# Optimization experiments

Measured on AMD Instinct MI355X. Metric: run time of the kernel, lower is better.

## Reference

```python
import jax, jax.numpy as jnp
import numpy as np

B, T, D, H = 2, 2048, 1024, 16
HD = D // H  # head dim = 64

def setup_inputs() -> dict:
    key = jax.random.key(0)
    k1, k2, k3 = jax.random.split(key, 3)
    x = jax.random.normal(k1, (B, T, D), dtype=jnp.float32)
    W_qkv = jax.random.normal(k2, (D, 3 * D), dtype=jnp.float32) * 0.02
    b_qkv = jax.random.normal(k3, (3 * D,), dtype=jnp.float32) * 0.02
    return {"x": x, "W_qkv": W_qkv, "b_qkv": b_qkv}

def reference(x, W_qkv, b_qkv):
    Bc, Tc, C = x.shape
    qkv = x @ W_qkv + b_qkv                     # [B,T,3D]
    q, k, v = jnp.split(qkv, 3, axis=-1)        # each [B,T,D]
    def to_heads(t):
        return t.reshape(Bc, Tc, H, HD).transpose(0, 2, 1, 3)  # [B,H,T,hd]
    q, k, v = to_heads(q), to_heads(k), to_heads(v)
    scale = 1.0 / jnp.sqrt(jnp.asarray(HD, dtype=x.dtype))
    att = jnp.einsum('bhqd,bhkd->bhqk', q, k) * scale  # [B,H,T,T]
    att = jax.nn.softmax(att, axis=-1)
    y = jnp.einsum('bhqk,bhkd->bhqd', att, v)          # [B,H,T,hd]
    return y.transpose(0, 2, 1, 3).reshape(Bc, Tc, C)
```

## Files before the change

### kernel.cpp

```cpp
#include <hip/hip_runtime.h>
#include <cstdint>

typedef unsigned short u16;
typedef __bf16 bf16x8 __attribute__((ext_vector_type(8)));
typedef float f32x4 __attribute__((ext_vector_type(4)));
typedef u16 u16x4 __attribute__((ext_vector_type(4)));
typedef u16 u16x8 __attribute__((ext_vector_type(8)));

static __device__ __forceinline__ u16 f2bf(float f) {
  return __builtin_bit_cast(u16, (__bf16)f);
}
static __device__ __forceinline__ float fexp2(float x) {
  float r;
  asm("v_exp_f32 %0, %1" : "=v"(r) : "v"(x));
  return r;
}

#define GLOAD16(gsrc, ldst) \
  __builtin_amdgcn_global_load_lds((const __attribute__((address_space(1))) void*)(gsrc), \
                                   (__attribute__((address_space(3))) void*)(ldst), 16, 0, 0)


__global__ __launch_bounds__(256) void k_prep(const float* __restrict__ x,
                                              const float* __restrict__ W,
                                              u16* __restrict__ xbf,
                                              u16* __restrict__ Wt) {
  __shared__ __align__(16) u16 tile[64 * 72];
  int t = threadIdx.x;
  if (blockIdx.x < 2048) {
    int idx = blockIdx.x * 256 + t;
    const float4* xv = (const float4*)x;
    float4 a = xv[(size_t)idx * 2];
    float4 b = xv[(size_t)idx * 2 + 1];
    u16x8 o;
    o[0]=f2bf(a.x); o[1]=f2bf(a.y); o[2]=f2bf(a.z); o[3]=f2bf(a.w);
    o[4]=f2bf(b.x); o[5]=f2bf(b.y); o[6]=f2bf(b.z); o[7]=f2bf(b.w);
    *(u16x8*)(xbf + (size_t)idx * 8) = o;
    return;
  }
  int bid = blockIdx.x - 2048;
  int bk = bid & 15, bn = bid >> 4;
  int k0 = bk * 64, n0 = bn * 64;
  #pragma unroll
  for (int r = 0; r < 4; r++) {
    int id = r * 256 + t;
    int kl = id >> 4;
    int c  = (id & 15) * 4;
    float4 v = *(const float4*)(W + (size_t)(k0 + kl) * 3072 + n0 + c);
    u16x4 o; o[0]=f2bf(v.x); o[1]=f2bf(v.y); o[2]=f2bf(v.z); o[3]=f2bf(v.w);
    *(u16x4*)(tile + kl * 72 + c) = o;
  }
  __syncthreads();
  #pragma unroll
  for (int r = 0; r < 2; r++) {
    int id = r * 256 + t;
    int nl = id >> 3;
    int w  = id & 7;
    u16x8 o;
    #pragma unroll
    for (int i = 0; i < 8; i++) o[i] = tile[(w * 8 + i) * 72 + nl];
    *(u16x8*)(Wt + (size_t)(n0 + nl) * 1024 + k0 + w * 8) = o;
  }
}

__global__ __launch_bounds__(256, 2) void k_gemm_qkv(const u16* __restrict__ xbf,
                                                     const u16* __restrict__ wt,
                                                     const float* __restrict__ bias,
                                                     u16* __restrict__ qkv,
                                                     u16* __restrict__ vT) {
  __shared__ __align__(16) u16 As[2 * 128 * 64];
  __shared__ __align__(16) u16 Bs[2 * 192 * 64];
  int wg = blockIdx.x;
  int swz = (wg & 7) * 64 + (wg >> 3);
  int mt = swz >> 4, nt = swz & 15;
  int m0 = mt * 128, n0 = nt * 192;
  int t = threadIdx.x;
  int lane = t & 63, wid = t >> 6;
  int wm = wid >> 1, wn = wid & 1;
  int g = lane >> 4, li = lane & 15;

  f32x4 acc[4][6];
  #pragma unroll
  for (int i = 0; i < 4; i++)
    #pragma unroll
    for (int j = 0; j < 6; j++) acc[i][j] = (f32x4){0.f, 0.f, 0.f, 0.f};

  auto stage = [&](int kt, int buf) {
    char* ad = (char*)As + buf * 16384;
    char* bd = (char*)Bs + buf * 24576;
    #pragma unroll
    for (int i = 0; i < 4; i++) {
      int p = t + i * 256;
      int row = p >> 3, ug = (p & 7) ^ (row & 7);
      GLOAD16(xbf + (size_t)(m0 + row) * 1024 + kt * 64 + ug * 8, ad + p * 16);
    }
    #pragma unroll
    for (int i = 0; i < 6; i++) {
      int p = t + i * 256;
      int row = p >> 3, ug = (p & 7) ^ (row & 7);
      GLOAD16(wt + (size_t)(n0 + row) * 1024 + kt * 64 + ug * 8, bd + p * 16);
    }
  };

  stage(0, 0);
  for (int kt = 0; kt < 16; ++kt) {
    __syncthreads();
    if (kt < 15) stage(kt + 1, (kt & 1) ^ 1);
    const char* ab = (const char*)As + (kt & 1) * 16384;
    const char* bb = (const char*)Bs + (kt & 1) * 24576;

    #pragma unroll
    for (int kk = 0; kk < 2; ++kk) {
      bf16x8 af[4], bfr[6];
      #pragma unroll
      for (int mi = 0; mi < 4; mi++) {
        int row = wm * 64 + mi * 16 + li;
        int u = (kk * 4 + g) ^ (row & 7);
        af[mi] = *(const bf16x8*)(ab + row * 128 + u * 16);
      }
      #pragma unroll
      for (int ni = 0; ni < 6; ni++) {
        int row = wn * 96 + ni * 16 + li;
        int u = (kk * 4 + g) ^ (row & 7);
        bfr[ni] = *(const bf16x8*)(bb + row * 128 + u * 16);
      }
      __builtin_amdgcn_s_setprio(1);
      #pragma unroll
      for (int mi = 0; mi < 4; mi++)
        #pragma unroll
        for (int ni = 0; ni < 6; ni++)
          acc[mi][ni] = __builtin_amdgcn_mfma_f32_16x16x32_bf16(af[mi], bfr[ni], acc[mi][ni], 0, 0, 0);
      __builtin_amdgcn_s_setprio(0);
    }
  }

  int b = m0 >> 11;
  int tbase = m0 & 2047;
  #pragma unroll
  for (int ni = 0; ni < 6; ni++) {
    int col = n0 + wn * 96 + ni * 16 + li;
    float bv = bias[col];
    float sc = (col < 1024) ? 0.18033688011112042f : 1.0f;
    #pragma unroll
    for (int mi = 0; mi < 4; mi++) {
      int trow = tbase + wm * 64 + mi * 16 + g * 4;
      if (col < 2048) {
        #pragma unroll
        for (int j = 0; j < 4; j++) {
          float v = (acc[mi][ni][j] + bv) * sc;
          qkv[(size_t)(b * 2048 + trow + j) * 3072 + col] = f2bf(v);
        }
      } else {
        u16x4 o;
        #pragma unroll
        for (int j = 0; j < 4; j++) o[j] = f2bf(acc[mi][ni][j] + bv);
        *(u16x4*)(vT + ((size_t)(b * 1024 + (col - 2048))) * 2048 + trow) = o;
      }
    }
  }
}

__global__ __launch_bounds__(128, 4) void k_attn(const u16* __restrict__ qkv,
                                                 const u16* __restrict__ vT,
                                                 float* __restrict__ out) {
  __shared__ __align__(16) u16 smem[16384];
  int bid = blockIdx.x;
  int bh = bid & 31, qt = bid >> 5;
  int b = bh >> 4, h = bh & 15;
  int qbase = qt * 64;
  int t = threadIdx.x, lane = t & 63, wave = t >> 6;
  int g = lane >> 4, li = lane & 15;

  size_t qrowa = (size_t)(b * 2048 + qbase + wave * 32 + li) * 3072 + h * 64;
  bf16x8 qa0 = *(const bf16x8*)(qkv + qrowa + g * 8);
  bf16x8 qa1 = *(const bf16x8*)(qkv + qrowa + 32 + g * 8);
  bf16x8 qb0 = *(const bf16x8*)(qkv + qrowa + 16 * 3072 + g * 8);
  bf16x8 qb1 = *(const bf16x8*)(qkv + qrowa + 16 * 3072 + 32 + g * 8);

  u16x8 ob;
  #pragma unroll
  for (int i = 0; i < 8; i++) ob[i] = 0x3F80;
  bf16x8 ones = __builtin_bit_cast(bf16x8, ob);

  f32x4 o[2][4];
  #pragma unroll
  for (int f = 0; f < 2; f++)
    #pragma unroll
    for (int i = 0; i < 4; i++) o[f][i] = (f32x4){0.f, 0.f, 0.f, 0.f};
  f32x4 la = (f32x4){0.f, 0.f, 0.f, 0.f}, lb = la;

  const u16* kbase_g = qkv + (size_t)(b * 2048) * 3072 + 1024 + h * 64;
  const u16* vbase_g = vT + (size_t)(bh * 64) * 2048;

  int kRow[4], kUg[4], vRow[4], vUg[4];
  #pragma unroll
  for (int i = 0; i < 4; i++) {
    int p = t + i * 128;
    int kr = p >> 3;
    kRow[i] = (kr & 32) | ((kr & 16) >> 2) | (((kr >> 2) & 3) << 3) | (kr & 3);
    kUg[i] = (p & 7) ^ (kr & 7);
    vRow[i] = kr;
    vUg[i] = (p & 7) ^ (kr & 7);
  }

  auto stage = [&](int key0, int buf) {
    char* kd = (char*)smem + buf * 8192;
    char* vd_ = (char*)smem + 16384 + buf * 8192;
    #pragma unroll
    for (int i = 0; i < 4; i++) {
      int p = t + i * 128;
      GLOAD16(kbase_g + (size_t)(key0 + kRow[i]) * 3072 + kUg[i] * 8, kd + p * 16);
      GLOAD16(vbase_g + (size_t)vRow[i] * 2048 + key0 + vUg[i] * 8, vd_ + p * 16);
    }
  };

  stage(0, 0);
  asm volatile("s_waitcnt vmcnt(0)" ::: "memory");
  __syncthreads();

  #pragma unroll 2
  for (int ph = 0; ph < 32; ++ph) {
    int buf = ph & 1;
    const char* kb = (const char*)smem + buf * 8192;
    const char* vb = (const char*)smem + 16384 + buf * 8192;

    if (ph < 31) stage((ph + 1) * 64, buf ^ 1);

    f32x4 sa[4], sb[4];
    int u0 = g ^ (li & 7);
    __builtin_amdgcn_s_setprio(1);
    #pragma unroll
    for (int st = 0; st < 4; ++st) {
      bf16x8 kf0 = *(const bf16x8*)(kb + (st * 16 + li) * 128 + u0 * 16);
      bf16x8 kf1 = *(const bf16x8*)(kb + (st * 16 + li) * 128 + (u0 ^ 4) * 16);
      f32x4 z = (f32x4){0.f, 0.f, 0.f, 0.f};
      sa[st] = __builtin_amdgcn_mfma_f32_16x16x32_bf16(kf0, qa0, z, 0, 0, 0);
      sa[st] = __builtin_amdgcn_mfma_f32_16x16x32_bf16(kf1, qa1, sa[st], 0, 0, 0);
      sb[st] = __builtin_amdgcn_mfma_f32_16x16x32_bf16(kf0, qb0, z, 0, 0, 0);
      sb[st] = __builtin_amdgcn_mfma_f32_16x16x32_bf16(kf1, qb1, sb[st], 0, 0, 0);
    }
    __builtin_amdgcn_s_setprio(0);

    float pa[16], pbf[16];
    #pragma unroll
    for (int i = 0; i < 16; i++) pa[i] = fexp2(sa[i >> 2][i & 3]);
    #pragma unroll
    for (int i = 0; i < 16; i++) pbf[i] = fexp2(sb[i >> 2][i & 3]);

    bf16x8 pba[2], pbb[2];
    #pragma unroll
    for (int c = 0; c < 2; c++)
      #pragma unroll
      for (int e = 0; e < 8; e++) {
        pba[c][e] = (__bf16)pa[c * 8 + e];
        pbb[c][e] = (__bf16)pbf[c * 8 + e];
      }

    __builtin_amdgcn_s_setprio(1);
    la = __builtin_amdgcn_mfma_f32_16x16x32_bf16(ones, pba[0], la, 0, 0, 0);
    la = __builtin_amdgcn_mfma_f32_16x16x32_bf16(ones, pba[1], la, 0, 0, 0);
    lb = __builtin_amdgcn_mfma_f32_16x16x32_bf16(ones, pbb[0], lb, 0, 0, 0);
    lb = __builtin_amdgcn_mfma_f32_16x16x32_bf16(ones, pbb[1], lb, 0, 0, 0);
    #pragma unroll
    for (int c = 0; c < 2; c++) {
      int uc = c * 4 + g;
      #pragma unroll
      for (int dt = 0; dt < 4; dt++) {
        int d = dt * 16 + li;
        bf16x8 vf = *(const bf16x8*)(vb + d * 128 + ((uc ^ (d & 7)) << 4));
        o[0][dt] = __builtin_amdgcn_mfma_f32_16x16x32_bf16(vf, pba[c], o[0][dt], 0, 0, 0);
        o[1][dt] = __builtin_amdgcn_mfma_f32_16x16x32_bf16(vf, pbb[c], o[1][dt], 0, 0, 0);
      }
    }
    __builtin_amdgcn_s_setprio(0);

    __syncthreads();
  }

  float inva = 1.0f / la[0], invb = 1.0f / lb[0];
  #pragma unroll
  for (int f = 0; f < 2; f++) {
    float inv = f ? invb : inva;
    int ql = wave * 32 + f * 16 + li;
    #pragma unroll
    for (int dt = 0; dt < 4; dt++) {
      int u = dt * 4 + g;
      int up = u ^ (ql & 7);
      f32x4 v = o[f][dt] * inv;
      *(f32x4*)((char*)smem + ql * 256 + up * 16) = v;
    }
  }
  __syncthreads();
  int ql = t >> 1, seg = t & 1;
  size_t obase = (size_t)(b * 2048 + qbase + ql) * 1024 + h * 64;
  #pragma unroll
  for (int i = 0; i < 8; i++) {
    int u = seg * 8 + i;
    int up = u ^ (ql & 7);
    f32x4 v = *(const f32x4*)((const char*)smem + ql * 256 + up * 16);
    *(f32x4*)(out + obase + u * 4) = v;
  }
}

extern "C" void kernel_launch(void* const* d_in, const int* in_sizes, int n_in,
                              void* d_out, int out_size, void* d_ws, size_t ws_size,
                              hipStream_t stream) {
  const float* x    = (const float*)d_in[0];
  const float* W    = (const float*)d_in[1];
  const float* bias = (const float*)d_in[2];
  float* out = (float*)d_out;
  char* ws = (char*)d_ws;
  u16* xbf = (u16*)(ws + 0);
  u16* wt  = (u16*)(ws + 8388608);
  u16* qkv = (u16*)(ws + 14680064);
  u16* vt  = (u16*)(ws + 39845888);

  k_prep<<<2816, 256, 0, stream>>>(x, W, xbf, wt);
  k_gemm_qkv<<<512, 256, 0, stream>>>(xbf, wt, bias, qkv, vt);
  k_attn<<<1024, 128, 0, stream>>>(qkv, vt, out);
}
```

Before: 93.15 us.

## Split KV sequence across wave pairs with 128-query tiles in attention kernel

The attention kernel moves to 256-thread blocks covering 128 queries, with each wave holding 64 queries (four 16-row fragments) so each K/V LDS fragment feeds more MFMAs. The key range is split in two halves handled by different wave pairs, giving 16 iterations instead of 32. Partial outputs and row sums are merged through shared memory at the end. This is meant to raise arithmetic reuse per LDS load and halve the loop trip count, at the cost of more registers (o[4][4], s[4][4]), lower occupancy, and a final reduction step.

```diff
diff --git a/kernel.cpp b/kernel.cpp
--- a/kernel.cpp
+++ b/kernel.cpp
@@ -160,57 +160,64 @@
   }
 }
 
-__global__ __launch_bounds__(128, 4) void k_attn(const u16* __restrict__ qkv,
+__global__ __launch_bounds__(256, 2) void k_attn(const u16* __restrict__ qkv,
                                                  const u16* __restrict__ vT,
                                                  float* __restrict__ out) {
-  __shared__ __align__(16) u16 smem[16384];
+  __shared__ __align__(16) u16 smem[32768];
   int bid = blockIdx.x;
   int bh = bid & 31, qt = bid >> 5;
   int b = bh >> 4, h = bh & 15;
-  int qbase = qt * 64;
+  int qbase = qt * 128;
   int t = threadIdx.x, lane = t & 63, wave = t >> 6;
   int g = lane >> 4, li = lane & 15;
-
-  size_t qrowa = (size_t)(b * 2048 + qbase + wave * 32 + li) * 3072 + h * 64;
-  bf16x8 qa0 = *(const bf16x8*)(qkv + qrowa + g * 8);
-  bf16x8 qa1 = *(const bf16x8*)(qkv + qrowa + 32 + g * 8);
-  bf16x8 qb0 = *(const bf16x8*)(qkv + qrowa + 16 * 3072 + g * 8);
-  bf16x8 qb1 = *(const bf16x8*)(qkv + qrowa + 16 * 3072 + 32 + g * 8);
+  int kvHalf = wave >> 1, qh = wave & 1;
+
+  bf16x8 q[4][2];
+  #pragma unroll
+  for (int qf = 0; qf < 4; qf++) {
+    size_t qrow = (size_t)(b * 2048 + qbase + qh * 64 + qf * 16 + li) * 3072 + h * 64;
+    q[qf][0] = *(const bf16x8*)(qkv + qrow + g * 8);
+    q[qf][1] = *(const bf16x8*)(qkv + qrow + 32 + g * 8);
+  }
 
   u16x8 ob;
   #pragma unroll
   for (int i = 0; i < 8; i++) ob[i] = 0x3F80;
   bf16x8 ones = __builtin_bit_cast(bf16x8, ob);
 
-  f32x4 o[2][4];
-  #pragma unroll
-  for (int f = 0; f < 2; f++)
-    #pragma unroll
-    for (int i = 0; i < 4; i++) o[f][i] = (f32x4){0.f, 0.f, 0.f, 0.f};
-  f32x4 la = (f32x4){0.f, 0.f, 0.f, 0.f}, lb = la;
+  f32x4 o[4][4];
+  #pragma unroll
+  for (int i = 0; i < 4; i++)
+    #pragma unroll
+    for (int j = 0; j < 4; j++) o[i][j] = (f32x4){0.f, 0.f, 0.f, 0.f};
+  f32x4 la[4];
+  #pragma unroll
+  for (int i = 0; i < 4; i++) la[i] = (f32x4){0.f, 0.f, 0.f, 0.f};
 
   const u16* kbase_g = qkv + (size_t)(b * 2048) * 3072 + 1024 + h * 64;
   const u16* vbase_g = vT + (size_t)(bh * 64) * 2048;
 
-  int kRow[4], kUg[4], vRow[4], vUg[4];
+  int kR[4], kU[4];
+  size_t vO[4];
   #pragma unroll
   for (int i = 0; i < 4; i++) {
-    int p = t + i * 128;
-    int kr = p >> 3;
-    kRow[i] = (kr & 32) | ((kr & 16) >> 2) | (((kr >> 2) & 3) << 3) | (kr & 3);
-    kUg[i] = (p & 7) ^ (kr & 7);
-    vRow[i] = kr;
-    vUg[i] = (p & 7) ^ (kr & 7);
+    int p = t + i * 256;
+    int hf = p >> 9, p9 = p & 511;
+    int kr = p9 >> 3;
+    kR[i] = hf * 1024 + ((kr & 32) | ((kr & 16) >> 2) | (((kr >> 2) & 3) << 3) | (kr & 3));
+    kU[i] = (p9 & 7) ^ (kr & 7);
+    int d = p9 >> 3, u = p9 & 7;
+    vO[i] = (size_t)d * 2048 + hf * 1024 + ((u ^ (d & 7)) * 8);
   }
 
   auto stage = [&](int key0, int buf) {
-    char* kd = (char*)smem + buf * 8192;
-    char* vd_ = (char*)smem + 16384 + buf * 8192;
+    char* kd = (char*)smem + buf * 32768;
+    char* vd = kd + 16384;
     #pragma unroll
     for (int i = 0; i < 4; i++) {
-      int p = t + i * 128;
-      GLOAD16(kbase_g + (size_t)(key0 + kRow[i]) * 3072 + kUg[i] * 8, kd + p * 16);
-      GLOAD16(vbase_g + (size_t)vRow[i] * 2048 + key0 + vUg[i] * 8, vd_ + p * 16);
+      int p = t + i * 256;
+      GLOAD16(kbase_g + (size_t)(key0 + kR[i]) * 3072 + kU[i] * 8, kd + p * 16);
+      GLOAD16(vbase_g + vO[i] + key0, vd + p * 16);
     }
   };
 
@@ -218,58 +225,56 @@
   asm volatile("s_waitcnt vmcnt(0)" ::: "memory");
   __syncthreads();
 
-  #pragma unroll 2
-  for (int ph = 0; ph < 32; ++ph) {
-    int buf = ph & 1;
-    const char* kb = (const char*)smem + buf * 8192;
-    const char* vb = (const char*)smem + 16384 + buf * 8192;
-
-    if (ph < 31) stage((ph + 1) * 64, buf ^ 1);
-
-    f32x4 sa[4], sb[4];
+  for (int ph = 0; ph < 16; ++ph) {
+    const char* bufb = (const char*)smem + (ph & 1) * 32768;
+    const char* kb = bufb + kvHalf * 8192;
+    const char* vb = bufb + 16384 + kvHalf * 8192;
+
+    if (ph < 15) stage((ph + 1) * 64, (ph & 1) ^ 1);
+
+    f32x4 s[4][4];
     int u0 = g ^ (li & 7);
     __builtin_amdgcn_s_setprio(1);
     #pragma unroll
     for (int st = 0; st < 4; ++st) {
       bf16x8 kf0 = *(const bf16x8*)(kb + (st * 16 + li) * 128 + u0 * 16);
       bf16x8 kf1 = *(const bf16x8*)(kb + (st * 16 + li) * 128 + (u0 ^ 4) * 16);
-      f32x4 z = (f32x4){0.f, 0.f, 0.f, 0.f};
-      sa[st] = __builtin_amdgcn_mfma_f32_16x16x32_bf16(kf0, qa0, z, 0, 0, 0);
-      sa[st] = __builtin_amdgcn_mfma_f32_16x16x32_bf16(kf1, qa1, sa[st], 0, 0, 0);
-      sb[st] = __builtin_amdgcn_mfma_f32_16x16x32_bf16(kf0, qb0, z, 0, 0, 0);
-      sb[st] = __builtin_amdgcn_mfma_f32_16x16x32_bf16(kf1, qb1, sb[st], 0, 0, 0);
+      #pragma unroll
+      for (int qf = 0; qf < 4; qf++) {
+        f32x4 z = (f32x4){0.f, 0.f, 0.f, 0.f};
+        s[st][qf] = __builtin_amdgcn_mfma_f32_16x16x32_bf16(kf0, q[qf][0], z, 0, 0, 0);
+        s[st][qf] = __builtin_amdgcn_mfma_f32_16x16x32_bf16(kf1, q[qf][1], s[st][qf], 0, 0, 0);
+      }
     }
     __builtin_amdgcn_s_setprio(0);
 
-    float pa[16], pbf[16];
-    #pragma unroll
-    for (int i = 0; i < 16; i++) pa[i] = fexp2(sa[i >> 2][i & 3]);
-    #pragma unroll
-    for (int i = 0; i < 16; i++) pbf[i] = fexp2(sb[i >> 2][i & 3]);
-
-    bf16x8 pba[2], pbb[2];
-    #pragma unroll
-    for (int c = 0; c < 2; c++)
-      #pragma unroll
-      for (int e = 0; e < 8; e++) {
-        pba[c][e] = (__bf16)pa[c * 8 + e];
-        pbb[c][e] = (__bf16)pbf[c * 8 + e];
-      }
+    bf16x8 pb[4][2];
+    #pragma unroll
+    for (int qf = 0; qf < 4; qf++) {
+      float p16[16];
+      #pragma unroll
+      for (int i = 0; i < 16; i++) p16[i] = fexp2(s[i >> 2][qf][i & 3]);
+      #pragma unroll
+      for (int c = 0; c < 2; c++)
+        #pragma unroll
+        for (int e = 0; e < 8; e++) pb[qf][c][e] = (__bf16)p16[c * 8 + e];
+    }
 
     __builtin_amdgcn_s_setprio(1);
-    la = __builtin_amdgcn_mfma_f32_16x16x32_bf16(ones, pba[0], la, 0, 0, 0);
-    la = __builtin_amdgcn_mfma_f32_16x16x32_bf16(ones, pba[1], la, 0, 0, 0);
-    lb = __builtin_amdgcn_mfma_f32_16x16x32_bf16(ones, pbb[0], lb, 0, 0, 0);
-    lb = __builtin_amdgcn_mfma_f32_16x16x32_bf16(ones, pbb[1], lb, 0, 0, 0);
+    #pragma unroll
+    for (int qf = 0; qf < 4; qf++) {
+      la[qf] = __builtin_amdgcn_mfma_f32_16x16x32_bf16(ones, pb[qf][0], la[qf], 0, 0, 0);
+      la[qf] = __builtin_amdgcn_mfma_f32_16x16x32_bf16(ones, pb[qf][1], la[qf], 0, 0, 0);
+    }
     #pragma unroll
     for (int c = 0; c < 2; c++) {
-      int uc = c * 4 + g;
       #pragma unroll
       for (int dt = 0; dt < 4; dt++) {
         int d = dt * 16 + li;
-        bf16x8 vf = *(const bf16x8*)(vb + d * 128 + ((uc ^ (d & 7)) << 4));
-        o[0][dt] = __builtin_amdgcn_mfma_f32_16x16x32_bf16(vf, pba[c], o[0][dt], 0, 0, 0);
-        o[1][dt] = __builtin_amdgcn_mfma_f32_16x16x32_bf16(vf, pbb[c], o[1][dt], 0, 0, 0);
+        bf16x8 vf = *(const bf16x8*)(vb + d * 128 + (((c * 4 + g) ^ (d & 7)) << 4));
+        #pragma unroll
+        for (int qf = 0; qf < 4; qf++)
+          o[qf][dt] = __builtin_amdgcn_mfma_f32_16x16x32_bf16(vf, pb[qf][c], o[qf][dt], 0, 0, 0);
       }
     }
     __builtin_amdgcn_s_setprio(0);
@@ -277,28 +282,35 @@
     __syncthreads();
   }
 
-  float inva = 1.0f / la[0], invb = 1.0f / lb[0];
-  #pragma unroll
-  for (int f = 0; f < 2; f++) {
-    float inv = f ? invb : inva;
-    int ql = wave * 32 + f * 16 + li;
-    #pragma unroll
-    for (int dt = 0; dt < 4; dt++) {
-      int u = dt * 4 + g;
-      int up = u ^ (ql & 7);
-      f32x4 v = o[f][dt] * inv;
-      *(f32x4*)((char*)smem + ql * 256 + up * 16) = v;
+  float* pO = (float*)smem;
+  float* pL = (float*)((char*)smem + 32768);
+  if (kvHalf) {
+    #pragma unroll
+    for (int qf = 0; qf < 4; qf++) {
+      int qq = qh * 64 + qf * 16 + li;
+      #pragma unroll
+      for (int dt = 0; dt < 4; dt++) {
+        int u = dt * 4 + g;
+        *(f32x4*)((char*)pO + qq * 256 + ((u ^ (qq & 7)) << 4)) = o[qf][dt];
+      }
+      if (g == 0) pL[qq] = la[qf][0];
     }
   }
   __syncthreads();
-  int ql = t >> 1, seg = t & 1;
-  size_t obase = (size_t)(b * 2048 + qbase + ql) * 1024 + h * 64;
-  #pragma unroll
-  for (int i = 0; i < 8; i++) {
-    int u = seg * 8 + i;
-    int up = u ^ (ql & 7);
-    f32x4 v = *(const f32x4*)((const char*)smem + ql * 256 + up * 16);
-    *(f32x4*)(out + obase + u * 4) = v;
+  if (!kvHalf) {
+    #pragma unroll
+    for (int qf = 0; qf < 4; qf++) {
+      int qq = qh * 64 + qf * 16 + li;
+      float inv = 1.0f / (la[qf][0] + pL[qq]);
+      size_t orow = (size_t)(b * 2048 + qbase + qq) * 1024 + h * 64;
+      #pragma unroll
+      for (int dt = 0; dt < 4; dt++) {
+        int u = dt * 4 + g;
+        f32x4 p2 = *(const f32x4*)((const char*)pO + qq * 256 + ((u ^ (qq & 7)) << 4));
+        f32x4 r = (o[qf][dt] + p2) * inv;
+        *(f32x4*)(out + orow + u * 4) = r;
+      }
+    }
   }
 }
 
@@ -317,5 +329,5 @@
 
   k_prep<<<2816, 256, 0, stream>>>(x, W, xbf, wt);
   k_gemm_qkv<<<512, 256, 0, stream>>>(xbf, wt, bias, qkv, vt);
-  k_attn<<<1024, 128, 0, stream>>>(qkv, vt, out);
-}
+  k_attn<<<512, 256, 0, stream>>>(qkv, vt, out);
+}
```

Result: faster. 81.76 us (-12.2%).
